# Performance work log

Measured on AMD Instinct MI355X. Metric: run time of the kernel, lower is better.

Reference implementation:

```python
import jax, jax.numpy as jnp
from jax import lax
import numpy as np
import math

A = 9          # anchors per location
NC = 80        # classes
SCORE_T = 0.05
NMS_T = 0.5
DPI = 100      # detections_per_img (also per-level K in _inference)
BBOX_CLIP = math.log(1000.0 / 16.0)
LEVEL_SHAPES = [(64, 64), (32, 32), (16, 16), (8, 8)]
STRIDES = [8, 16, 32, 64]
BASE_SIZES = [32, 64, 128, 256]


def _conv(x, w, b):
    y = lax.conv_general_dilated(x, w, (1, 1), 'SAME', dimension_numbers=('NCHW', 'OIHW', 'NCHW'))
    return y + b[None, :, None, None]


def _head(feats, tower_w, tower_b, out_w, out_b, out_dim):
    outs = []
    for f in feats:
        x = f
        for i in range(tower_w.shape[0]):
            x = jax.nn.relu(_conv(x, tower_w[i], tower_b[i]))
        x = _conv(x, out_w, out_b)                     # [B, A*out_dim, H, W]
        B, _, H, W = x.shape
        x = x.reshape(B, A, out_dim, H, W).transpose(0, 3, 4, 1, 2).reshape(B, H * W * A, out_dim)
        outs.append(x)
    return outs


def _clip_boxes(b, img_h, img_w):
    x1 = jnp.clip(b[:, 0], 0.0, float(img_w)); y1 = jnp.clip(b[:, 1], 0.0, float(img_h))
    x2 = jnp.clip(b[:, 2], 0.0, float(img_w)); y2 = jnp.clip(b[:, 3], 0.0, float(img_h))
    return jnp.stack([x1, y1, x2, y2], axis=-1)


def _level_anchors(H, W, stride, s, img_h, img_w):
    # torchvision AnchorGenerator: sizes (s, s*2^(1/3), s*2^(2/3)), ratios (0.5,1,2)
    sizes = jnp.array([s, int(s * 2 ** (1 / 3)), int(s * 2 ** (2 / 3))], dtype=jnp.float32)
    ratios = jnp.array([0.5, 1.0, 2.0], dtype=jnp.float32)
    h_r = jnp.sqrt(ratios); w_r = 1.0 / h_r
    ws = (w_r[:, None] * sizes[None, :]).reshape(-1)
    hs = (h_r[:, None] * sizes[None, :]).reshape(-1)
    base = jnp.round(jnp.stack([-ws, -hs, ws, hs], axis=-1) / 2.0)   # [9,4]
    sx = (jnp.arange(W) * stride).astype(jnp.float32)
    sy = (jnp.arange(H) * stride).astype(jnp.float32)
    yy, xx = jnp.meshgrid(sy, sx, indexing='ij')
    shifts = jnp.stack([xx, yy, xx, yy], axis=-1).reshape(-1, 1, 4)   # [H*W,1,4]
    anch = (shifts + base[None]).reshape(-1, 4)                        # [H*W*A,4]
    return _clip_boxes(anch, img_h, img_w)


def _decode(rel, anch):
    # BoxCoder.decode_single with weights (1,1,1,1)
    w = anch[:, 2] - anch[:, 0]; h = anch[:, 3] - anch[:, 1]
    cx = anch[:, 0] + 0.5 * w;   cy = anch[:, 1] + 0.5 * h
    dx, dy = rel[:, 0], rel[:, 1]
    dw = jnp.minimum(rel[:, 2], BBOX_CLIP)
    dh = jnp.minimum(rel[:, 3], BBOX_CLIP)
    pcx = dx * w + cx; pcy = dy * h + cy
    pw = jnp.exp(dw) * w; ph = jnp.exp(dh) * h
    return jnp.stack([pcx - 0.5 * pw, pcy - 0.5 * ph, pcx + 0.5 * pw, pcy + 0.5 * ph], axis=-1)


def _pairwise_iou(boxes):
    area = (boxes[:, 2] - boxes[:, 0]) * (boxes[:, 3] - boxes[:, 1])
    lt = jnp.maximum(boxes[:, None, :2], boxes[None, :, :2])
    rb = jnp.minimum(boxes[:, None, 2:], boxes[None, :, 2:])
    wh = jnp.clip(rb - lt, 0.0)
    inter = wh[..., 0] * wh[..., 1]
    return inter / (area[:, None] + area[None, :] - inter + 1e-9)


def _per_image(logits, regs, anchors, img_h, img_w):
    bs, ss, ls = [], [], []
    for logit, reg, anch in zip(logits, regs, anchors):
        scores = jax.nn.sigmoid(logit).reshape(-1)                   # [N*NC]
        masked = jnp.where(scores > SCORE_T, scores, -1.0)
        top_s, idx = lax.top_k(masked, DPI)                          # fixed K = detections_per_img
        aidx = idx // NC
        lbl = idx % NC
        boxes = _clip_boxes(_decode(reg[aidx], anch[aidx]), img_h, img_w)
        valid = top_s > SCORE_T
        bs.append(boxes)
        ss.append(jnp.where(valid, top_s, -1.0))
        ls.append(jnp.where(valid, lbl, -1))
    boxes = jnp.concatenate(bs, 0); scores = jnp.concatenate(ss, 0); labels = jnp.concatenate(ls, 0)
    # batched (per-class) NMS via label coordinate offsets
    order = jnp.argsort(-scores)
    boxes_s = boxes[order]; scores_s = scores[order]; labels_s = labels[order]
    offset = labels_s.astype(boxes.dtype) * (float(max(img_h, img_w)) + 1.0)
    iou = lax.stop_gradient(_pairwise_iou(boxes_s + offset[:, None]))
    N = scores_s.shape[0]
    ar = jnp.arange(N)
    def body(i, keep):
        sup = keep[i] & (iou[i] > NMS_T) & (ar > i)
        return keep & ~sup
    keep = lax.fori_loop(0, N, body, scores_s > SCORE_T)
    fs, fi = lax.top_k(jnp.where(keep, scores_s, -1.0), DPI)
    ok = fs > SCORE_T
    fb = jnp.where(ok[:, None], boxes_s[fi], 0.0)
    fl = jnp.where(ok, labels_s[fi], -1)
    fs = jnp.where(ok, fs, 0.0)
    return fb, fs, fl


def setup_inputs() -> dict:
    key = jax.random.key(0)
    ks = jax.random.split(key, 8)
    B = 4
    w_scale = 0.04
    inp = {}
    shapes = [(B, 256, 64, 64), (B, 256, 32, 32), (B, 256, 16, 16), (B, 256, 8, 8)]
    for i, sh in enumerate(shapes):
        inp[f'f{i}'] = jax.random.normal(ks[i], sh, dtype=jnp.float32)
    inp['cls_tower_w'] = jax.random.normal(ks[4], (4, 256, 256, 3, 3), dtype=jnp.float32) * w_scale
    inp['cls_tower_b'] = jnp.zeros((4, 256), dtype=jnp.float32)
    inp['cls_out_w'] = jax.random.normal(ks[5], (A * NC, 256, 3, 3), dtype=jnp.float32) * w_scale
    inp['cls_out_b'] = jnp.full((A * NC,), -2.0, dtype=jnp.float32)  # prior-like bias
    inp['reg_tower_w'] = jax.random.normal(ks[6], (4, 256, 256, 3, 3), dtype=jnp.float32) * w_scale
    inp['reg_tower_b'] = jnp.zeros((4, 256), dtype=jnp.float32)
    inp['reg_out_w'] = jax.random.normal(ks[7], (A * 4, 256, 3, 3), dtype=jnp.float32) * w_scale
    inp['reg_out_b'] = jnp.zeros((A * 4,), dtype=jnp.float32)
    inp['image_h'] = 512
    inp['image_w'] = 512
    return inp


def reference(f0, f1, f2, f3, cls_tower_w, cls_tower_b, cls_out_w, cls_out_b,
              reg_tower_w, reg_tower_b, reg_out_w, reg_out_b, image_h, image_w):
    feats = [f0, f1, f2, f3]
    cls_logits = _head(feats, cls_tower_w, cls_tower_b, cls_out_w, cls_out_b, NC)   # list of [B,Ni,NC]
    bbox_regs = _head(feats, reg_tower_w, reg_tower_b, reg_out_w, reg_out_b, 4)     # list of [B,Ni,4]
    anchors = [_level_anchors(H, W, st, s, image_h, image_w)
               for (H, W), st, s in zip(LEVEL_SHAPES, STRIDES, BASE_SIZES)]
    fn = lambda ls, rs: _per_image(ls, rs, anchors, image_h, image_w)
    boxes, scores, labels = jax.vmap(fn)(tuple(cls_logits), tuple(bbox_regs))
    return boxes, scores, labels
```

## Files before the change

### kernel.cpp

```cpp
#include <hip/hip_runtime.h>
#include <math.h>

#define A_NUM 9
#define NCLS 80
#define IMG_KEY 3916800
#define IMG_REG 195840
#define CAP 8192
#define HBINS 16384

#define CHUNK_SLOTS 24064
#define CHUNK_BYTES (CHUNK_SLOTS * 16)
#define ACT_SLAB ((size_t)CHUNK_BYTES * 16)
#define WCHUNK_BYTES 40960
#define WCOG_BYTES (WCHUNK_BYTES * 16)

typedef _Float16 h8 __attribute__((ext_vector_type(8)));
typedef float fx4 __attribute__((ext_vector_type(4)));
typedef unsigned short u16;

__constant__ int   c_W[4]       = {64, 32, 16, 8};
__constant__ int   c_stride[4]  = {8, 16, 32, 64};
__constant__ float c_sizes[4][3]= {{32.f,40.f,50.f},{64.f,80.f,101.f},{128.f,161.f,203.f},{256.f,322.f,406.f}};
__constant__ int   c_keyOff[4]  = {0, 2949120, 3686400, 3870720};
__constant__ int   c_keyCnt[4]  = {2949120, 737280, 184320, 46080};
__constant__ int   c_regOff[4]  = {0, 147456, 184320, 193536};
__constant__ int   c_C[4]       = {66, 34, 18, 18};
__constant__ int   c_lvlSlot[4] = {0, 17424, 22048, 23344};
__constant__ int   c_pOff[4]    = {0, 1024, 1280, 1344};

__device__ __forceinline__ void gl_lds16(const void* g, void* l) {
    __builtin_amdgcn_global_load_lds(
        (const __attribute__((address_space(1))) void*)g,
        (__attribute__((address_space(3))) void*)l, 16, 0, 0);
}

__global__ __launch_bounds__(256) void pad16_k(
    const float* __restrict__ f0, const float* __restrict__ f1,
    const float* __restrict__ f2, const float* __restrict__ f3,
    char* __restrict__ Pin)
{
    int idx = blockIdx.x * 256 + threadIdx.x;
    const int PER_IMG = 16 * 2 * 1360;
    if (idx >= 4 * PER_IMG) return;
    int img = idx / PER_IMG;
    int r = idx - img * PER_IMG;
    int chunk = r / (2 * 1360);
    int r2 = r - chunk * (2 * 1360);
    int hfsel = r2 / 1360;
    int p = r2 - hfsel * 1360;
    int lvl = (p < 1024) ? 0 : (p < 1280 ? 1 : (p < 1344 ? 2 : 3));
    int u = p - c_pOff[lvl];
    int sh = 4 - lvl;
    int y = u >> sh;
    int xg = u & ((1 << sh) - 1);
    int x0 = xg * 4;
    int W = 64 >> lvl;
    const float* f = (lvl == 0) ? f0 : (lvl == 1) ? f1 : (lvl == 2) ? f2 : f3;
    int ci0 = chunk * 16 + hfsel * 8;
    float4 v[8];
    #pragma unroll
    for (int j = 0; j < 8; ++j)
        v[j] = *reinterpret_cast<const float4*>(
            f + ((size_t)(img * 256 + ci0 + j)) * (W * W) + y * W + x0);
    char* base = Pin + (size_t)img * ACT_SLAB + (size_t)chunk * CHUNK_BYTES;
    const int C = c_C[lvl];
    size_t rowSlot = (size_t)c_lvlSlot[lvl] + (size_t)((y + 1) * 4 + hfsel) * C;
    #pragma unroll
    for (int c = 0; c < 4; ++c) {
        h8 hv, lv;
        #pragma unroll
        for (int j = 0; j < 8; ++j) {
            float val = (c == 0) ? v[j].x : (c == 1) ? v[j].y : (c == 2) ? v[j].z : v[j].w;
            _Float16 hh = (_Float16)val;
            hv[j] = hh;
            lv[j] = (_Float16)(val - (float)hh);
        }
        size_t slot = rowSlot + (x0 + c + 1);
        *reinterpret_cast<h8*>(base + slot * 16) = hv;
        *reinterpret_cast<h8*>(base + (slot + 2 * (size_t)C) * 16) = lv;
    }
}

__global__ __launch_bounds__(256) void repack16_k(
    const float* __restrict__ src, u16* __restrict__ dst,
    int C_out, int nCg, int total)
{
    int idx = blockIdx.x * 256 + threadIdx.x;
    if (idx >= total) return;
    int per = nCg * 16 * 1280;
    int layer = idx / per;
    int r = idx - layer * per;
    int cg = r / (16 * 1280);
    int r2 = r - cg * (16 * 1280);
    int chunk = r2 / 1280;
    int s = r2 - chunk * 1280;
    int co = s & 63;
    int r3 = s >> 6;
    int hfsel = r3 & 1;
    int kk = r3 >> 1;
    int coG = cg * 64 + co;
    float v[8];
    if (kk < 9 && coG < C_out) {
        const float* sp = src + ((size_t)(layer * C_out + coG)) * 2304
                        + (size_t)(chunk * 16 + hfsel * 8) * 9 + kk;
        #pragma unroll
        for (int j = 0; j < 8; ++j) v[j] = sp[j * 9];
    } else {
        #pragma unroll
        for (int j = 0; j < 8; ++j) v[j] = 0.f;
    }
    h8 hv, lv;
    #pragma unroll
    for (int j = 0; j < 8; ++j) {
        _Float16 hh = (_Float16)v[j];
        hv[j] = hh;
        lv[j] = (_Float16)(v[j] - (float)hh);
    }
    size_t e = ((size_t)((layer * nCg + cg) * 16 + chunk)) * 20480
             + (size_t)(kk >> 1) * 4096 + (size_t)(kk & 1) * 2048
             + (size_t)hfsel * 512 + (size_t)co * 8;
    *reinterpret_cast<h8*>(dst + e) = hv;
    *reinterpret_cast<h8*>(dst + e + 1024) = lv;
}

__global__ __launch_bounds__(256, 3) void conv16(
    const char* __restrict__ Pin, const char* __restrict__ bufIn, char* __restrict__ bufOut,
    const u16* __restrict__ repA, const float* __restrict__ bA,
    const u16* __restrict__ repB, const float* __restrict__ bB,
    unsigned* __restrict__ keys, float* __restrict__ regb,
    int mode, int usePin)
{
    const int tid = threadIdx.x;
    const int lane = tid & 63;
    const int wv = tid >> 6;
    const int t43 = blockIdx.x;

    int img, head, coBase, C_out, epi;
    if (mode == 0) {
        img = blockIdx.z & 3; head = blockIdx.z >> 2;
        coBase = blockIdx.y * 64; C_out = 256; epi = 0;
    } else {
        img = blockIdx.z;
        if (blockIdx.y < 12) { head = 0; coBase = blockIdx.y * 64; C_out = 720; epi = 1; }
        else                 { head = 1; coBase = 0;               C_out = 36;  epi = 2; }
    }
    const float* bsel = head ? bB : bA;
    const u16* wsel = head ? repB : repA;
    const char* wBase = (const char*)wsel + (size_t)(coBase >> 6) * WCOG_BYTES;

    int lvl, ty, tx;
    if (t43 < 32)      { lvl = 0; ty = t43 >> 2; tx = t43 & 3; }
    else if (t43 < 40) { int u = t43 - 32; lvl = 1; ty = u >> 1; tx = u & 1; }
    else if (t43 < 42) { lvl = 2; ty = t43 - 40; tx = 0; }
    else               { lvl = 3; ty = 0; tx = 0; }
    const int W = 64 >> lvl;
    const int C = c_C[lvl];
    const int tileY = ty * 8, tileX = tx * 16;

    const char* srcB = usePin ? Pin + (size_t)img * ACT_SLAB
                              : bufIn + (size_t)(head * 4 + img) * ACT_SLAB;

    __shared__ alignas(16) char sA[11520];
    __shared__ alignas(16) char sB[40960];

    const int laneCol = lane & 15;
    const int g = lane >> 4;
    const int halfS = g & 1;
    const int tapS = g >> 1;
    int laneA[5];
    #pragma unroll
    for (int k = 0; k < 5; ++k) {
        int kk = 2 * k + tapS; if (kk > 8) kk = 8;
        int ky = kk / 3;
        int kx = kk - ky * 3;
        laneA[k] = ky * 1152 + halfS * 288 + (laneCol + kx) * 16;
    }
    const int laneB = tapS * 4096 + halfS * 1024 + laneCol * 16;

    size_t aSrc[3]; int aDst[3]; bool aOk[3];
    #pragma unroll
    for (int p = 0; p < 3; ++p) {
        int s = tid + 256 * p;
        aOk[p] = (s < 720);
        int sc = aOk[p] ? s : 719;
        int row = sc / 72;
        int q = sc - row * 72;
        int pl = q / 36;
        int q2 = q - pl * 36;
        int hf = q2 / 18;
        int col = q2 - hf * 18;
        aSrc[p] = (size_t)(c_lvlSlot[lvl] + ((tileY + row) * 4 + pl * 2 + hf) * C
                           + tileX + col) * 16;
        aDst[p] = sc * 16;
    }

    fx4 acc[2][4];
    #pragma unroll
    for (int mt = 0; mt < 2; ++mt)
        #pragma unroll
        for (int nt = 0; nt < 4; ++nt)
            acc[mt][nt] = (fx4){0.f, 0.f, 0.f, 0.f};

    #pragma unroll 1
    for (int ck = 0; ck < 16; ++ck) {
        int4 av[3];
        const char* srcCk = srcB + (size_t)ck * CHUNK_BYTES;
        #pragma unroll
        for (int p = 0; p < 3; ++p)
            if (aOk[p]) av[p] = *reinterpret_cast<const int4*>(srcCk + aSrc[p]);
        const char* wCk = wBase + (size_t)ck * WCHUNK_BYTES;
        for (int j = wv; j < 40; j += 4)
            gl_lds16(wCk + j * 1024 + lane * 16, (char*)sB + j * 1024);
        #pragma unroll
        for (int p = 0; p < 3; ++p)
            if (aOk[p]) *reinterpret_cast<int4*>(sA + aDst[p]) = av[p];
        __syncthreads();

        #pragma unroll
        for (int k = 0; k < 5; ++k) {
            const char* bk = sB + k * 8192;
            h8 Bh[4], Bl[4];
            #pragma unroll
            for (int nt = 0; nt < 4; ++nt) {
                Bh[nt] = *reinterpret_cast<const h8*>(bk + nt * 256 + laneB);
                Bl[nt] = *reinterpret_cast<const h8*>(bk + 2048 + nt * 256 + laneB);
            }
            #pragma unroll
            for (int mt = 0; mt < 2; ++mt) {
                const char* am = sA + (wv * 2 + mt) * 1152 + laneA[k];
                h8 Ah = *reinterpret_cast<const h8*>(am);
                h8 Al = *reinterpret_cast<const h8*>(am + 576);
                #pragma unroll
                for (int nt = 0; nt < 4; ++nt) {
                    acc[mt][nt] = __builtin_amdgcn_mfma_f32_16x16x32_f16(Ah, Bh[nt], acc[mt][nt], 0, 0, 0);
                    acc[mt][nt] = __builtin_amdgcn_mfma_f32_16x16x32_f16(Ah, Bl[nt], acc[mt][nt], 0, 0, 0);
                    acc[mt][nt] = __builtin_amdgcn_mfma_f32_16x16x32_f16(Al, Bh[nt], acc[mt][nt], 0, 0, 0);
                }
            }
        }
        __syncthreads();
    }

    const int HW = W * W;
    if (epi == 0) {
        char* dstB = bufOut + (size_t)(head * 4 + img) * ACT_SLAB;
        #pragma unroll
        for (int mt = 0; mt < 2; ++mt) {
            int y = tileY + wv * 2 + mt;
            int gy4 = (y + 1) * 4;
            #pragma unroll
            for (int nt = 0; nt < 4; ++nt) {
                int coG = coBase + nt * 16 + laneCol;
                float b = bsel[coG];
                size_t sBase = (size_t)(coG >> 4) * CHUNK_SLOTS + c_lvlSlot[lvl]
                             + (size_t)(gy4 + ((coG >> 3) & 1)) * C;
                int ci8 = coG & 7;
                #pragma unroll
                for (int i = 0; i < 4; ++i) {
                    int x = tileX + g * 4 + i;
                    if (x >= W) continue;
                    float v = fmaxf(acc[mt][nt][i] + b, 0.f);
                    _Float16 hh = (_Float16)v;
                    _Float16 ll = (_Float16)(v - (float)hh);
                    size_t slot = sBase + (x + 1);
                    *reinterpret_cast<_Float16*>(dstB + slot * 16 + ci8 * 2) = hh;
                    *reinterpret_cast<_Float16*>(dstB + (slot + 2 * (size_t)C) * 16 + ci8 * 2) = ll;
                }
            }
        }
    } else if (epi == 1) {
        unsigned* kb = keys + (size_t)img * IMG_KEY + c_keyOff[lvl];
        #pragma unroll
        for (int mt = 0; mt < 2; ++mt) {
            int y = tileY + wv * 2 + mt;
            int x0 = tileX + g * 4;
            if (x0 >= W) continue;
            #pragma unroll
            for (int nt = 0; nt < 4; ++nt) {
                int coG = coBase + nt * 16 + laneCol;
                if (coG >= C_out) continue;
                float b = bsel[coG];
                unsigned kq[4];
                #pragma unroll
                for (int i = 0; i < 4; ++i) {
                    float sc = 1.0f / (1.0f + expf(-(acc[mt][nt][i] + b)));
                    kq[i] = (sc > 0.05f) ? __float_as_uint(sc) : 0u;
                }
                *reinterpret_cast<uint4*>(kb + (size_t)coG * HW + y * W + x0) =
                    make_uint4(kq[0], kq[1], kq[2], kq[3]);
            }
        }
    } else {
        float* rb = regb + (size_t)img * IMG_REG + c_regOff[lvl];
        #pragma unroll
        for (int mt = 0; mt < 2; ++mt) {
            int y = tileY + wv * 2 + mt;
            #pragma unroll
            for (int nt = 0; nt < 4; ++nt) {
                int coG = nt * 16 + laneCol;
                if (coG >= C_out) continue;
                float b = bsel[coG];
                int a = coG >> 2, jj = coG & 3;
                #pragma unroll
                for (int i = 0; i < 4; ++i) {
                    int x = tileX + g * 4 + i;
                    if (x >= W) continue;
                    rb[((size_t)(y * W + x) * A_NUM + a) * 4 + jj] = acc[mt][nt][i] + b;
                }
            }
        }
    }
}

__global__ __launch_bounds__(256) void hist_k(const unsigned* __restrict__ keys,
                                              unsigned* __restrict__ hist)
{
    int il = blockIdx.y, img = il >> 2, lvl = il & 3;
    int n = c_keyCnt[lvl];
    int chunk = blockIdx.x * 16384;
    if (chunk >= n) return;
    __shared__ unsigned h[HBINS];
    for (int t = threadIdx.x; t < HBINS; t += 256) h[t] = 0;
    __syncthreads();
    const uint4* k4 = (const uint4*)(keys + (size_t)img * IMG_KEY + c_keyOff[lvl]);
    int i0 = chunk >> 2, i1 = min(chunk + 16384, n) >> 2;
    for (int i = i0 + (int)threadIdx.x; i < i1; i += 256) {
        uint4 kv = k4[i];
        if (kv.x) atomicAdd(&h[kv.x >> 18], 1u);
        if (kv.y) atomicAdd(&h[kv.y >> 18], 1u);
        if (kv.z) atomicAdd(&h[kv.z >> 18], 1u);
        if (kv.w) atomicAdd(&h[kv.w >> 18], 1u);
    }
    __syncthreads();
    unsigned* gh = hist + (size_t)il * HBINS;
    for (int t = threadIdx.x; t < HBINS; t += 256)
        if (h[t]) atomicAdd(&gh[t], h[t]);
}

__global__ __launch_bounds__(256) void thresh_k(const unsigned* __restrict__ hist,
                                                unsigned* __restrict__ tbin)
{
    const unsigned* h = hist + (size_t)blockIdx.x * HBINS;
    __shared__ unsigned cs[256];
    int tid = threadIdx.x;
    unsigned s = 0;
    int base = tid * 64;
    for (int q = 0; q < 64; ++q) { int b = base + q; if (b >= 1) s += h[b]; }
    cs[tid] = s;
    __syncthreads();
    if (tid == 0) {
        unsigned total = 0, sel = 0;
        for (int c = 255; c >= 0; --c) {
            if (total + cs[c] >= 100u) {
                int lo = (c == 0) ? 1 : c * 64;
                for (int b = c * 64 + 63; b >= lo; --b) {
                    total += h[b];
                    if (total >= 100u) { sel = (unsigned)b; break; }
                }
                break;
            }
            total += cs[c];
        }
        tbin[blockIdx.x] = sel;
    }
}

__global__ __launch_bounds__(256) void compact_k(const unsigned* __restrict__ keys,
                                                 const unsigned* __restrict__ tbin,
                                                 unsigned* __restrict__ cnt,
                                                 uint2* __restrict__ comp)
{
    int il = blockIdx.y, img = il >> 2, lvl = il & 3;
    int n = c_keyCnt[lvl];
    int chunk = blockIdx.x * 16384;
    if (chunk >= n) return;
    const uint4* k4 = (const uint4*)(keys + (size_t)img * IMG_KEY + c_keyOff[lvl]);
    unsigned thr = tbin[il] << 18;
    int shift = 12 - 2 * lvl;
    int hwm = (1 << shift) - 1;
    int i0 = chunk >> 2, i1 = min(chunk + 16384, n) >> 2;
    __shared__ unsigned lcnt, lbase, lcur;
    if (threadIdx.x == 0) { lcnt = 0; lcur = 0; }
    __syncthreads();
    unsigned myc = 0;
    for (int i = i0 + (int)threadIdx.x; i < i1; i += 256) {
        uint4 kv = k4[i];
        myc += (kv.x != 0u && kv.x >= thr);
        myc += (kv.y != 0u && kv.y >= thr);
        myc += (kv.z != 0u && kv.z >= thr);
        myc += (kv.w != 0u && kv.w >= thr);
    }
    if (myc) atomicAdd(&lcnt, myc);
    __syncthreads();
    if (threadIdx.x == 0 && lcnt) lbase = atomicAdd(&cnt[il], lcnt);
    __syncthreads();
    if (lcnt == 0) return;
    uint2* c = comp + (size_t)il * CAP;
    for (int i = i0 + (int)threadIdx.x; i < i1; i += 256) {
        uint4 kv = k4[i];
        unsigned kk[4] = {kv.x, kv.y, kv.z, kv.w};
        #pragma unroll
        for (int j = 0; j < 4; ++j) {
            unsigned key = kk[j];
            if (key != 0u && key >= thr) {
                int t = i * 4 + j;
                int co = t >> shift, p = t & hwm;
                int a = co / NCLS, cls = co - a * NCLS;
                unsigned idx = (unsigned)((p * A_NUM + a) * NCLS + cls);
                unsigned pos = lbase + atomicAdd(&lcur, 1u);
                if (pos < CAP) c[pos] = make_uint2(key, idx);
            }
        }
    }
}

__global__ __launch_bounds__(256) void topsort_k(const unsigned* __restrict__ cnt,
                                                 const uint2* __restrict__ comp,
                                                 uint2* __restrict__ topk)
{
    __shared__ unsigned long long s[CAP];
    int il = blockIdx.x, tid = threadIdx.x;
    int n = (int)min(cnt[il], (unsigned)CAP);
    const uint2* c = comp + (size_t)il * CAP;
    for (int i = tid; i < CAP; i += 256) {
        unsigned long long v = 0ull;
        if (i < n) {
            uint2 e = c[i];
            v = ((unsigned long long)e.x << 32) | (unsigned long long)(~e.y);
        }
        s[i] = v;
    }
    for (int k = 2; k <= CAP; k <<= 1) {
        for (int j = k >> 1; j > 0; j >>= 1) {
            __syncthreads();
            for (int p = tid; p < CAP / 2; p += 256) {
                int i = ((p & ~(j - 1)) << 1) | (p & (j - 1));
                int ixj = i | j;
                unsigned long long a = s[i], b = s[ixj];
                if (((i & k) == 0) ? (a < b) : (a > b)) { s[i] = b; s[ixj] = a; }
            }
        }
    }
    __syncthreads();
    if (tid < 100) {
        unsigned long long v = s[tid];
        topk[il * 100 + tid] = make_uint2((unsigned)(v >> 32), ~(unsigned)(v & 0xFFFFFFFFull));
    }
}

__global__ void decode_k(const uint2* __restrict__ topk, const float* __restrict__ regb,
                         float* __restrict__ cboxes, float* __restrict__ cscores,
                         int* __restrict__ clabels, const int* __restrict__ ph, const int* __restrict__ pw)
{
    int il = blockIdx.x, img = il >> 2, lvl = il & 3;
    int j = threadIdx.x;
    if (j >= 100) return;
    float imgW = (float)pw[0], imgH = (float)ph[0];
    uint2 tk = topk[il * 100 + j];
    int outP = img * 400 + lvl * 100 + j;
    if (tk.x == 0u) {
        cboxes[outP * 4 + 0] = 0.f; cboxes[outP * 4 + 1] = 0.f;
        cboxes[outP * 4 + 2] = 0.f; cboxes[outP * 4 + 3] = 0.f;
        cscores[outP] = -1.0f; clabels[outP] = -1;
        return;
    }
    float score = __uint_as_float(tk.x);
    unsigned idx = tk.y;
    int aidx = (int)(idx / NCLS);
    int lbl  = (int)(idx - (unsigned)aidx * NCLS);
    int a = aidx % A_NUM, p = aidx / A_NUM;
    int W = c_W[lvl];
    int y = p / W, x = p - y * W;
    int r = a / 3, si = a - r * 3;
    float ratio = (r == 0) ? 0.5f : ((r == 1) ? 1.0f : 2.0f);
    float size = c_sizes[lvl][si];
    float hr = sqrtf(ratio);
    float wr = 1.0f / hr;
    float wsz = wr * size, hsz = hr * size;
    float bw = rintf(wsz * 0.5f), bh = rintf(hsz * 0.5f);
    float sx = (float)(x * c_stride[lvl]), sy = (float)(y * c_stride[lvl]);
    float ax1 = fminf(fmaxf(sx - bw, 0.f), imgW);
    float ay1 = fminf(fmaxf(sy - bh, 0.f), imgH);
    float ax2 = fminf(fmaxf(sx + bw, 0.f), imgW);
    float ay2 = fminf(fmaxf(sy + bh, 0.f), imgH);
    float aw = ax2 - ax1, ah = ay2 - ay1;
    float cx = ax1 + 0.5f * aw, cy = ay1 + 0.5f * ah;
    const float* rel = regb + (size_t)img * IMG_REG + c_regOff[lvl] + (size_t)aidx * 4;
    float dx = rel[0], dy = rel[1];
    float dw = fminf(rel[2], 4.135166556742356f);
    float dh = fminf(rel[3], 4.135166556742356f);
    float pcx = dx * aw + cx, pcy = dy * ah + cy;
    float pwd = expf(dw) * aw, phd = expf(dh) * ah;
    float x1 = pcx - 0.5f * pwd, y1 = pcy - 0.5f * phd;
    float x2 = pcx + 0.5f * pwd, y2 = pcy + 0.5f * phd;
    cboxes[outP * 4 + 0] = fminf(fmaxf(x1, 0.f), imgW);
    cboxes[outP * 4 + 1] = fminf(fmaxf(y1, 0.f), imgH);
    cboxes[outP * 4 + 2] = fminf(fmaxf(x2, 0.f), imgW);
    cboxes[outP * 4 + 3] = fminf(fmaxf(y2, 0.f), imgH);
    cscores[outP] = score;
    clabels[outP] = lbl;
}

__global__ __launch_bounds__(512) void nms_k(const float* __restrict__ cboxes,
                                             const float* __restrict__ cscores,
                                             const int* __restrict__ clabels,
                                             const int* __restrict__ ph, const int* __restrict__ pw,
                                             float* __restrict__ out)
{
    int img = blockIdx.x, tid = threadIdx.x;
    __shared__ float sSc[512];
    __shared__ int   sPos[512];
    __shared__ float bx1[400], by1[400], bx2[400], by2[400], sAr[400];
    __shared__ int   sKeep[400], sLbl[400];
    float imgH = (float)ph[0], imgW = (float)pw[0];
    float offm = fmaxf(imgH, imgW) + 1.0f;

    sSc[tid] = (tid < 400) ? cscores[img * 400 + tid] : -3.0f;
    sPos[tid] = tid;
    __syncthreads();

    for (int k = 2; k <= 512; k <<= 1) {
        for (int jj = k >> 1; jj > 0; jj >>= 1) {
            int ixj = tid ^ jj;
            if (ixj > tid) {
                float s1 = sSc[tid], s2 = sSc[ixj];
                int p1 = sPos[tid], p2 = sPos[ixj];
                bool bef = (s1 > s2) || (s1 == s2 && p1 < p2);
                bool sw = ((tid & k) == 0) ? (!bef) : bef;
                if (sw) { sSc[tid] = s2; sSc[ixj] = s1; sPos[tid] = p2; sPos[ixj] = p1; }
            }
            __syncthreads();
        }
    }

    if (tid < 400) {
        int p = sPos[tid];
        int lbl = clabels[img * 400 + p];
        float ofs = (float)lbl * offm;
        float x1 = cboxes[(img * 400 + p) * 4 + 0] + ofs;
        float y1 = cboxes[(img * 400 + p) * 4 + 1] + ofs;
        float x2 = cboxes[(img * 400 + p) * 4 + 2] + ofs;
        float y2 = cboxes[(img * 400 + p) * 4 + 3] + ofs;
        bx1[tid] = x1; by1[tid] = y1; bx2[tid] = x2; by2[tid] = y2;
        sAr[tid] = (x2 - x1) * (y2 - y1);
        sLbl[tid] = lbl;
        sKeep[tid] = (sSc[tid] > 0.05f) ? 1 : 0;
    }
    __syncthreads();

    for (int i = 0; i < 400; ++i) {
        if (sKeep[i]) {
            for (int j2 = i + 1 + tid; j2 < 400; j2 += 512) {
                float ltx = fmaxf(bx1[i], bx1[j2]), lty = fmaxf(by1[i], by1[j2]);
                float rbx = fminf(bx2[i], bx2[j2]), rby = fminf(by2[i], by2[j2]);
                float ww = fmaxf(rbx - ltx, 0.f), hh = fmaxf(rby - lty, 0.f);
                float inter = ww * hh;
                float iou = inter / (((sAr[i] + sAr[j2]) - inter) + 1e-9f);
                if (iou > 0.5f) sKeep[j2] = 0;
            }
        }
        __syncthreads();
    }

    if (tid == 0) {
        int rank = 0;
        for (int i = 0; i < 400 && rank < 100; ++i) {
            if (sKeep[i]) {
                int p = sPos[i];
                for (int kk = 0; kk < 4; ++kk)
                    out[(img * 100 + rank) * 4 + kk] = cboxes[(img * 400 + p) * 4 + kk];
                out[1600 + img * 100 + rank] = sSc[i];
                out[2000 + img * 100 + rank] = (float)sLbl[i];
                ++rank;
            }
        }
        for (; rank < 100; ++rank) {
            for (int kk = 0; kk < 4; ++kk) out[(img * 100 + rank) * 4 + kk] = 0.f;
            out[1600 + img * 100 + rank] = 0.f;
            out[2000 + img * 100 + rank] = -1.0f;
        }
    }
}

extern "C" void kernel_launch(void* const* d_in, const int* in_sizes, int n_in,
                              void* d_out, int out_size, void* d_ws, size_t ws_size,
                              hipStream_t stream)
{
    const float* f0 = (const float*)d_in[0];
    const float* f1 = (const float*)d_in[1];
    const float* f2 = (const float*)d_in[2];
    const float* f3 = (const float*)d_in[3];
    const float* cls_tw = (const float*)d_in[4];
    const float* cls_tb = (const float*)d_in[5];
    const float* cls_ow = (const float*)d_in[6];
    const float* cls_ob = (const float*)d_in[7];
    const float* reg_tw = (const float*)d_in[8];
    const float* reg_tb = (const float*)d_in[9];
    const float* reg_ow = (const float*)d_in[10];
    const float* reg_ob = (const float*)d_in[11];
    const int* ph = (const int*)d_in[12];
    const int* pw = (const int*)d_in[13];
    float* out = (float*)d_out;

    char* ws = (char*)d_ws;
    size_t off = 0;
    auto alloc = [&](size_t bytes) -> void* {
        void* p = ws + off;
        off = (off + bytes + 1023) & ~(size_t)1023;
        return p;
    };
    const size_t KEYS = (size_t)4 * IMG_KEY * 4;
    const size_t ACT8 = ACT_SLAB * 8;
    char*     Pin    = (char*)alloc(ACT_SLAB * 4 + 4096);
    char*     slabA  = (char*)alloc((KEYS > ACT8 ? KEYS : ACT8) + 4096);
    unsigned* keys   = (unsigned*)slabA;
    char*     actA   = slabA;
    char*     actB   = (char*)alloc(ACT8 + 4096);
    u16*      repCT  = (u16*)alloc((size_t)16 * WCOG_BYTES);
    u16*      repRT  = (u16*)alloc((size_t)16 * WCOG_BYTES);
    u16*      repCO  = (u16*)alloc((size_t)12 * WCOG_BYTES);
    u16*      repRO  = (u16*)alloc((size_t)1 * WCOG_BYTES);
    float*    regb   = (float*)alloc((size_t)4 * IMG_REG * 4);
    unsigned* hist   = (unsigned*)alloc((size_t)16 * HBINS * 4);
    unsigned* cnt    = (unsigned*)alloc(16 * 4);
    unsigned* tbin   = (unsigned*)alloc(16 * 4);
    uint2*    comp   = (uint2*)alloc((size_t)16 * CAP * 8);
    uint2*    topk   = (uint2*)alloc((size_t)1600 * 8);
    float*    cboxes = (float*)alloc((size_t)4 * 400 * 4 * 4);
    float*    cscores= (float*)alloc((size_t)4 * 400 * 4);
    int*      clabels= (int*)alloc((size_t)4 * 400 * 4);

    hipMemsetAsync(Pin, 0, ACT_SLAB * 4, stream);
    hipMemsetAsync(actA, 0, ACT8, stream);
    hipMemsetAsync(actB, 0, ACT8, stream);
    hipMemsetAsync(hist, 0, (size_t)16 * HBINS * 4, stream);
    hipMemsetAsync(cnt, 0, 64, stream);

    {
        int tPad = 4 * 16 * 2 * 1360;
        pad16_k<<<(tPad + 255) / 256, 256, 0, stream>>>(f0, f1, f2, f3, Pin);
        int tT = 4 * 4 * 16 * 1280;
        repack16_k<<<(tT + 255) / 256, 256, 0, stream>>>(cls_tw, repCT, 256, 4, tT);
        repack16_k<<<(tT + 255) / 256, 256, 0, stream>>>(reg_tw, repRT, 256, 4, tT);
        int tCO = 12 * 16 * 1280;
        repack16_k<<<(tCO + 255) / 256, 256, 0, stream>>>(cls_ow, repCO, 720, 12, tCO);
        int tRO = 16 * 1280;
        repack16_k<<<(tRO + 255) / 256, 256, 0, stream>>>(reg_ow, repRO, 36, 1, tRO);
    }

    const size_t RL = (size_t)4 * 16 * 20480;
    conv16<<<dim3(43, 4, 8), 256, 0, stream>>>(Pin, Pin, actA,
        repCT, cls_tb, repRT, reg_tb, keys, regb, 0, 1);
    conv16<<<dim3(43, 4, 8), 256, 0, stream>>>(Pin, actA, actB,
        repCT + RL, cls_tb + 256, repRT + RL, reg_tb + 256, keys, regb, 0, 0);
    conv16<<<dim3(43, 4, 8), 256, 0, stream>>>(Pin, actB, actA,
        repCT + 2 * RL, cls_tb + 512, repRT + 2 * RL, reg_tb + 512, keys, regb, 0, 0);
    conv16<<<dim3(43, 4, 8), 256, 0, stream>>>(Pin, actA, actB,
        repCT + 3 * RL, cls_tb + 768, repRT + 3 * RL, reg_tb + 768, keys, regb, 0, 0);
    conv16<<<dim3(43, 13, 4), 256, 0, stream>>>(Pin, actB, nullptr,
        repCO, cls_ob, repRO, reg_ob, keys, regb, 1, 0);

    hist_k<<<dim3(180, 16), 256, 0, stream>>>(keys, hist);
    thresh_k<<<16, 256, 0, stream>>>(hist, tbin);
    compact_k<<<dim3(180, 16), 256, 0, stream>>>(keys, tbin, cnt, comp);
    topsort_k<<<16, 256, 0, stream>>>(cnt, comp, topk);
    decode_k<<<16, 128, 0, stream>>>(topk, regb, cboxes, cscores, clabels, ph, pw);
    nms_k<<<4, 512, 0, stream>>>(cboxes, cscores, clabels, ph, pw, out);
}
```

Measured before the change: 1.526 ms.

## Enlarge conv tiles to 16x16, async LDS loads, XCD-aware block remap, staged epilogue

Doubles the conv spatial tile height from 8 to 16 rows so each block reuses its loaded weight chunk over twice as many output pixels, which halves weight traffic per output. Activation loads now go straight to LDS with the async global-to-LDS path instead of through registers. Blocks are linearised on a 1D grid and remapped by blockIdx mod 8, apparently so consecutive logical tiles are spread across the chip's dies. The tower epilogue stages results through LDS so each thread writes a 16-byte vector instead of scattered 2-byte stores. In exchange it adds more accumulator registers (occupancy hint drops from 3 to 2), extra syncthreads in the epilogue, wasted work on the padded small levels, and fewer blocks per launch.

```diff
diff --git a/kernel.cpp b/kernel.cpp
--- a/kernel.cpp
+++ b/kernel.cpp
@@ -123,7 +123,7 @@
     *reinterpret_cast<h8*>(dst + e + 1024) = lv;
 }
 
-__global__ __launch_bounds__(256, 3) void conv16(
+__global__ __launch_bounds__(256, 2) void conv16(
     const char* __restrict__ Pin, const char* __restrict__ bufIn, char* __restrict__ bufOut,
     const u16* __restrict__ repA, const float* __restrict__ bA,
     const u16* __restrict__ repB, const float* __restrict__ bB,
@@ -133,34 +133,44 @@
     const int tid = threadIdx.x;
     const int lane = tid & 63;
     const int wv = tid >> 6;
-    const int t43 = blockIdx.x;
-
-    int img, head, coBase, C_out, epi;
+
+    int img, head, coBase, C_out, epi, tile;
     if (mode == 0) {
-        img = blockIdx.z & 3; head = blockIdx.z >> 2;
-        coBase = blockIdx.y * 64; C_out = 256; epi = 0;
+        int hw = blockIdx.x;
+        int logical = (hw & 7) * 88 + (hw >> 3);
+        int z = logical / 88;
+        int rem = logical - z * 88;
+        tile = rem >> 2;
+        coBase = (rem & 3) * 64;
+        img = z & 3; head = z >> 2;
+        C_out = 256; epi = 0;
     } else {
-        img = blockIdx.z;
-        if (blockIdx.y < 12) { head = 0; coBase = blockIdx.y * 64; C_out = 720; epi = 1; }
-        else                 { head = 1; coBase = 0;               C_out = 36;  epi = 2; }
+        int hw = blockIdx.x;
+        int logical = (hw & 7) * 143 + (hw >> 3);
+        img = logical / 286;
+        int rem = logical - img * 286;
+        tile = rem / 13;
+        int yy = rem - tile * 13;
+        if (yy < 12) { head = 0; coBase = yy * 64; C_out = 720; epi = 1; }
+        else         { head = 1; coBase = 0;       C_out = 36;  epi = 2; }
     }
     const float* bsel = head ? bB : bA;
     const u16* wsel = head ? repB : repA;
     const char* wBase = (const char*)wsel + (size_t)(coBase >> 6) * WCOG_BYTES;
 
     int lvl, ty, tx;
-    if (t43 < 32)      { lvl = 0; ty = t43 >> 2; tx = t43 & 3; }
-    else if (t43 < 40) { int u = t43 - 32; lvl = 1; ty = u >> 1; tx = u & 1; }
-    else if (t43 < 42) { lvl = 2; ty = t43 - 40; tx = 0; }
-    else               { lvl = 3; ty = 0; tx = 0; }
+    if (tile < 16)      { lvl = 0; ty = tile >> 2; tx = tile & 3; }
+    else if (tile < 20) { int u = tile - 16; lvl = 1; ty = u >> 1; tx = u & 1; }
+    else if (tile == 20){ lvl = 2; ty = 0; tx = 0; }
+    else                { lvl = 3; ty = 0; tx = 0; }
     const int W = 64 >> lvl;
     const int C = c_C[lvl];
-    const int tileY = ty * 8, tileX = tx * 16;
+    const int tileY = ty * 16, tileX = tx * 16;
 
     const char* srcB = usePin ? Pin + (size_t)img * ACT_SLAB
                               : bufIn + (size_t)(head * 4 + img) * ACT_SLAB;
 
-    __shared__ alignas(16) char sA[11520];
+    __shared__ alignas(16) char sA[20736];
     __shared__ alignas(16) char sB[40960];
 
     const int laneCol = lane & 15;
@@ -177,43 +187,38 @@
     }
     const int laneB = tapS * 4096 + halfS * 1024 + laneCol * 16;
 
-    size_t aSrc[3]; int aDst[3]; bool aOk[3];
+    int aByte[6]; bool aOk[6];
     #pragma unroll
-    for (int p = 0; p < 3; ++p) {
+    for (int p = 0; p < 6; ++p) {
         int s = tid + 256 * p;
-        aOk[p] = (s < 720);
-        int sc = aOk[p] ? s : 719;
+        aOk[p] = (s < 1296);
+        int sc = aOk[p] ? s : 1295;
         int row = sc / 72;
         int q = sc - row * 72;
         int pl = q / 36;
         int q2 = q - pl * 36;
         int hf = q2 / 18;
         int col = q2 - hf * 18;
-        aSrc[p] = (size_t)(c_lvlSlot[lvl] + ((tileY + row) * 4 + pl * 2 + hf) * C
-                           + tileX + col) * 16;
-        aDst[p] = sc * 16;
-    }
-
-    fx4 acc[2][4];
+        aByte[p] = (c_lvlSlot[lvl] + ((tileY + row) * 4 + pl * 2 + hf) * C
+                    + tileX + col) * 16;
+    }
+
+    fx4 acc[4][4];
     #pragma unroll
-    for (int mt = 0; mt < 2; ++mt)
+    for (int mt = 0; mt < 4; ++mt)
         #pragma unroll
         for (int nt = 0; nt < 4; ++nt)
             acc[mt][nt] = (fx4){0.f, 0.f, 0.f, 0.f};
 
     #pragma unroll 1
     for (int ck = 0; ck < 16; ++ck) {
-        int4 av[3];
         const char* srcCk = srcB + (size_t)ck * CHUNK_BYTES;
         #pragma unroll
-        for (int p = 0; p < 3; ++p)
-            if (aOk[p]) av[p] = *reinterpret_cast<const int4*>(srcCk + aSrc[p]);
+        for (int p = 0; p < 6; ++p)
+            if (aOk[p]) gl_lds16(srcCk + aByte[p], (char*)sA + (wv * 64 + 256 * p) * 16);
         const char* wCk = wBase + (size_t)ck * WCHUNK_BYTES;
         for (int j = wv; j < 40; j += 4)
             gl_lds16(wCk + j * 1024 + lane * 16, (char*)sB + j * 1024);
-        #pragma unroll
-        for (int p = 0; p < 3; ++p)
-            if (aOk[p]) *reinterpret_cast<int4*>(sA + aDst[p]) = av[p];
         __syncthreads();
 
         #pragma unroll
@@ -226,8 +231,8 @@
                 Bl[nt] = *reinterpret_cast<const h8*>(bk + 2048 + nt * 256 + laneB);
             }
             #pragma unroll
-            for (int mt = 0; mt < 2; ++mt) {
-                const char* am = sA + (wv * 2 + mt) * 1152 + laneA[k];
+            for (int mt = 0; mt < 4; ++mt) {
+                const char* am = sA + (wv * 4 + mt) * 1152 + laneA[k];
                 h8 Ah = *reinterpret_cast<const h8*>(am);
                 h8 Al = *reinterpret_cast<const h8*>(am + 576);
                 #pragma unroll
@@ -244,37 +249,47 @@
     const int HW = W * W;
     if (epi == 0) {
         char* dstB = bufOut + (size_t)(head * 4 + img) * ACT_SLAB;
-        #pragma unroll
-        for (int mt = 0; mt < 2; ++mt) {
-            int y = tileY + wv * 2 + mt;
-            int gy4 = (y + 1) * 4;
+        _Float16* eW = reinterpret_cast<_Float16*>(sB + wv * 1024);
+        const int ci8 = laneCol & 7;
+        const int hf  = laneCol >> 3;
+        const int rpx = lane & 15, rhalf = (lane >> 4) & 1, rplane = lane >> 5;
+        const int rOff = rpx * 32 + rplane * 16 + rhalf * 8;
+        const int rx = tileX + rpx;
+        #pragma unroll
+        for (int mt = 0; mt < 4; ++mt) {
+            int y = tileY + wv * 4 + mt;
+            bool yok = (y < W);
             #pragma unroll
             for (int nt = 0; nt < 4; ++nt) {
                 int coG = coBase + nt * 16 + laneCol;
                 float b = bsel[coG];
-                size_t sBase = (size_t)(coG >> 4) * CHUNK_SLOTS + c_lvlSlot[lvl]
-                             + (size_t)(gy4 + ((coG >> 3) & 1)) * C;
-                int ci8 = coG & 7;
                 #pragma unroll
                 for (int i = 0; i < 4; ++i) {
-                    int x = tileX + g * 4 + i;
-                    if (x >= W) continue;
                     float v = fmaxf(acc[mt][nt][i] + b, 0.f);
                     _Float16 hh = (_Float16)v;
                     _Float16 ll = (_Float16)(v - (float)hh);
-                    size_t slot = sBase + (x + 1);
-                    *reinterpret_cast<_Float16*>(dstB + slot * 16 + ci8 * 2) = hh;
-                    *reinterpret_cast<_Float16*>(dstB + (slot + 2 * (size_t)C) * 16 + ci8 * 2) = ll;
+                    int px = g * 4 + i;
+                    eW[px * 32 + hf * 8 + ci8] = hh;
+                    eW[px * 32 + 16 + hf * 8 + ci8] = ll;
                 }
+                __syncthreads();
+                if (yok && rx < W) {
+                    int chunkIdx = (coBase + nt * 16) >> 4;
+                    size_t slot = (size_t)chunkIdx * CHUNK_SLOTS + c_lvlSlot[lvl]
+                                + (size_t)(((y + 1) * 2 + rplane) * 2 + rhalf) * C + (rx + 1);
+                    *reinterpret_cast<h8*>(dstB + slot * 16) =
+                        *reinterpret_cast<const h8*>(eW + rOff);
+                }
+                __syncthreads();
             }
         }
     } else if (epi == 1) {
         unsigned* kb = keys + (size_t)img * IMG_KEY + c_keyOff[lvl];
         #pragma unroll
-        for (int mt = 0; mt < 2; ++mt) {
-            int y = tileY + wv * 2 + mt;
+        for (int mt = 0; mt < 4; ++mt) {
+            int y = tileY + wv * 4 + mt;
             int x0 = tileX + g * 4;
-            if (x0 >= W) continue;
+            if (y >= W || x0 >= W) continue;
             #pragma unroll
             for (int nt = 0; nt < 4; ++nt) {
                 int coG = coBase + nt * 16 + laneCol;
@@ -293,8 +308,9 @@
     } else {
         float* rb = regb + (size_t)img * IMG_REG + c_regOff[lvl];
         #pragma unroll
-        for (int mt = 0; mt < 2; ++mt) {
-            int y = tileY + wv * 2 + mt;
+        for (int mt = 0; mt < 4; ++mt) {
+            int y = tileY + wv * 4 + mt;
+            if (y >= W) continue;
             #pragma unroll
             for (int nt = 0; nt < 4; ++nt) {
                 int coG = nt * 16 + laneCol;
@@ -611,11 +627,11 @@
     };
     const size_t KEYS = (size_t)4 * IMG_KEY * 4;
     const size_t ACT8 = ACT_SLAB * 8;
-    char*     Pin    = (char*)alloc(ACT_SLAB * 4 + 4096);
-    char*     slabA  = (char*)alloc((KEYS > ACT8 ? KEYS : ACT8) + 4096);
+    char*     Pin    = (char*)alloc(ACT_SLAB * 4 + 32768);
+    char*     slabA  = (char*)alloc((KEYS > ACT8 ? KEYS : ACT8) + 32768);
     unsigned* keys   = (unsigned*)slabA;
     char*     actA   = slabA;
-    char*     actB   = (char*)alloc(ACT8 + 4096);
+    char*     actB   = (char*)alloc(ACT8 + 32768);
     u16*      repCT  = (u16*)alloc((size_t)16 * WCOG_BYTES);
     u16*      repRT  = (u16*)alloc((size_t)16 * WCOG_BYTES);
     u16*      repCO  = (u16*)alloc((size_t)12 * WCOG_BYTES);
@@ -649,15 +665,15 @@
     }
 
     const size_t RL = (size_t)4 * 16 * 20480;
-    conv16<<<dim3(43, 4, 8), 256, 0, stream>>>(Pin, Pin, actA,
+    conv16<<<704, 256, 0, stream>>>(Pin, Pin, actA,
         repCT, cls_tb, repRT, reg_tb, keys, regb, 0, 1);
-    conv16<<<dim3(43, 4, 8), 256, 0, stream>>>(Pin, actA, actB,
+    conv16<<<704, 256, 0, stream>>>(Pin, actA, actB,
         repCT + RL, cls_tb + 256, repRT + RL, reg_tb + 256, keys, regb, 0, 0);
-    conv16<<<dim3(43, 4, 8), 256, 0, stream>>>(Pin, actB, actA,
+    conv16<<<704, 256, 0, stream>>>(Pin, actB, actA,
         repCT + 2 * RL, cls_tb + 512, repRT + 2 * RL, reg_tb + 512, keys, regb, 0, 0);
-    conv16<<<dim3(43, 4, 8), 256, 0, stream>>>(Pin, actA, actB,
+    conv16<<<704, 256, 0, stream>>>(Pin, actA, actB,
         repCT + 3 * RL, cls_tb + 768, repRT + 3 * RL, reg_tb + 768, keys, regb, 0, 0);
-    conv16<<<dim3(43, 13, 4), 256, 0, stream>>>(Pin, actB, nullptr,
+    conv16<<<1144, 256, 0, stream>>>(Pin, actB, nullptr,
         repCO, cls_ob, repRO, reg_ob, keys, regb, 1, 0);
 
     hist_k<<<dim3(180, 16), 256, 0, stream>>>(keys, hist);
```

Result: faster. 1.322 ms (-13.3%).
